# Kernel optimization log

Hardware: AMD Instinct MI355X
Metric: run time of the kernel (lower is better)

The kernel has to match this reference:

```python
import jax, jax.numpy as jnp
import numpy as np

B, P, E, V, H, NF = 256, 100, 32, 1000, 256, 33  # batch, pool, emb_size, vocab, hidden, n_embed_feats


def setup_inputs() -> dict:
    key = jax.random.key(0)
    k0, k1, k2, k3 = jax.random.split(key, 4)
    # integer-valued float tensor: cols 0,1 used raw; cols 2..34 cast to indices
    x = jax.random.randint(k0, (B, P, 35), 0, V).astype(jnp.float32)
    # 33 embedding tables stacked: [33, V, E]
    tables = jax.random.normal(k1, (NF, V, E), jnp.float32) * 0.02
    W1 = jax.random.normal(k2, (H, 35 * E), jnp.float32) * (1.0 / np.sqrt(35 * E))
    b1 = jnp.zeros((H,), jnp.float32)
    W2 = jax.random.normal(k3, (1, H), jnp.float32) * (1.0 / np.sqrt(H))
    b2 = jnp.zeros((1,), jnp.float32)
    return {"x": x, "tables": tables, "W1": W1, "b1": b1, "W2": W2, "b2": b2}


def reference(x, tables, W1, b1, W2, b2):
    b, p, _ = x.shape
    e = tables.shape[-1]
    # first 2 raw features repeated along embedding dim: [B,P,2,E]
    raw = jnp.repeat(x[:, :, :2, None], e, axis=3)
    # 33 embedding gathers, vectorized: tables[f, idx[...,f]] -> [B,P,33,E]
    idx = x[:, :, 2:].astype(jnp.int32)
    emb = tables[jnp.arange(NF)[None, None, :], idx]
    feat = jnp.concatenate([raw, emb], axis=2).reshape(b, p, 35 * e)
    h = jax.nn.relu(feat @ W1.T + b1)          # [B,P,256]
    logit = h @ W2.T + b2                       # [B,P,1]
    return jax.nn.softmax(logit, axis=1)        # softmax over pool dim
```

## Files before the change

### kernel.cpp

```cpp
#include <hip/hip_runtime.h>
#include <hip/hip_bf16.h>
#include <math.h>

#define BB 256
#define PP 100
#define EE 32
#define VV 1000
#define HH 256
#define NFF 33
#define F35 35
#define K1 1120
#define GSCALE 64.0f
#define GINV 0.015625f
#define NROWS (BB * PP)

#define FP8_HW 0
#if defined(__has_builtin)
#if __has_builtin(__builtin_amdgcn_cvt_pk_f32_fp8) && __has_builtin(__builtin_amdgcn_cvt_pk_fp8_f32)
#undef FP8_HW
#define FP8_HW 1
#endif
#endif

typedef float v2f __attribute__((ext_vector_type(2)));
typedef short bf16x8 __attribute__((ext_vector_type(8)));
typedef float f32x4 __attribute__((ext_vector_type(4)));

__device__ __forceinline__ unsigned char enc_fp8(float x) {
#if FP8_HW
    int pk = __builtin_amdgcn_cvt_pk_fp8_f32(x, 0.f, 0, false);
    return (unsigned char)(pk & 0xFF);
#else
    float a = fabsf(x);
    unsigned int s = (x < 0.f) ? 0x80u : 0u;
    if (a >= 448.f) return (unsigned char)(s | 0x7E);
    if (a < 0.015625f) {
        int m = (int)rintf(a * 512.f);
        if (m > 7) return (unsigned char)(s | 0x08);
        return (unsigned char)(s | (unsigned int)m);
    }
    unsigned int u = __float_as_uint(a);
    u += 0x00080000u;
    int e = (int)(u >> 23) - 127 + 7;
    if (e >= 16) return (unsigned char)(s | 0x7E);
    return (unsigned char)(s | ((unsigned int)e << 3) | ((u >> 20) & 7));
#endif
}

#if !FP8_HW
__device__ __forceinline__ float dec1(unsigned int b) {
    unsigned int s = b >> 7, e = (b >> 3) & 15, m = b & 7;
    float v = e ? __uint_as_float(((e + 120u) << 23) | (m << 20))
                : (float)m * 0.001953125f;
    return s ? -v : v;
}
#endif

__device__ __forceinline__ unsigned short f2bf(float x) {
    unsigned int b = __float_as_uint(x);
    return (unsigned short)((b + 0x7FFFu + ((b >> 16) & 1u)) >> 16);
}

__global__ __launch_bounds__(256) void k_pre(const float* __restrict__ tables,
                                             const float* __restrict__ W1,
                                             unsigned char* __restrict__ G,
                                             float* __restrict__ S01) {
    int bid = blockIdx.x;
    if (bid == NFF * 16) {
        int j = threadIdx.x;
        const float* row = W1 + (size_t)j * K1;
        float s0 = 0.f, s1 = 0.f;
#pragma unroll
        for (int e = 0; e < 32; ++e) { s0 += row[e]; s1 += row[32 + e]; }
        S01[j] = s0;
        S01[256 + j] = s1;
        return;
    }
    int f = bid % NFF;
    int rest = bid / NFF;
    int ctg = rest & 3;
    int vblk = rest >> 2;
    int t = threadIdx.x;
    int l = t & 63, w = t >> 6;
    int lr = l & 15, lg = l >> 4;

    const float* wp = W1 + (size_t)(ctg * 64 + w * 16 + lr) * K1 + 64 + 32 * f + lg * 4;
    float4 wa = *(const float4*)wp;
    float4 wb = *(const float4*)(wp + 16);
    bf16x8 afrag;
    afrag[0] = f2bf(wa.x); afrag[1] = f2bf(wa.y); afrag[2] = f2bf(wa.z); afrag[3] = f2bf(wa.w);
    afrag[4] = f2bf(wb.x); afrag[5] = f2bf(wb.y); afrag[6] = f2bf(wb.z); afrag[7] = f2bf(wb.w);

    __shared__ unsigned int stage[2][16][16];
    const f32x4 cz = {0.f, 0.f, 0.f, 0.f};

    for (int vt = 0; vt < 16; ++vt) {
        int v0 = vblk * 250 + vt * 16;
        int v = v0 + lr; if (v > VV - 1) v = VV - 1;
        const float* tp = tables + ((size_t)f * VV + v) * EE + lg * 4;
        float4 ta = *(const float4*)tp;
        float4 tb = *(const float4*)(tp + 16);
        bf16x8 bfrag;
        bfrag[0] = f2bf(ta.x); bfrag[1] = f2bf(ta.y); bfrag[2] = f2bf(ta.z); bfrag[3] = f2bf(ta.w);
        bfrag[4] = f2bf(tb.x); bfrag[5] = f2bf(tb.y); bfrag[6] = f2bf(tb.z); bfrag[7] = f2bf(tb.w);
        f32x4 d = __builtin_amdgcn_mfma_f32_16x16x32_bf16(afrag, bfrag, cz, 0, 0, 0);
        unsigned int pk;
#if FP8_HW
        int ipk = __builtin_amdgcn_cvt_pk_fp8_f32(d[0] * GSCALE, d[1] * GSCALE, 0, false);
        ipk = __builtin_amdgcn_cvt_pk_fp8_f32(d[2] * GSCALE, d[3] * GSCALE, ipk, true);
        pk = (unsigned int)ipk;
#else
        pk = (unsigned int)enc_fp8(d[0] * GSCALE) |
             ((unsigned int)enc_fp8(d[1] * GSCALE) << 8) |
             ((unsigned int)enc_fp8(d[2] * GSCALE) << 16) |
             ((unsigned int)enc_fp8(d[3] * GSCALE) << 24);
#endif
        stage[vt & 1][lr][w * 4 + lg] = pk;
        __syncthreads();
        if (t < 64) {
            int row = t >> 2, seg = t & 3;
            int vv = v0 + row;
            if (vv < VV) {
                uint4 val = *(const uint4*)&stage[vt & 1][row][seg * 4];
                *(uint4*)(G + ((size_t)f * VV + vv) * HH + ctg * 64 + seg * 16) = val;
            }
        }
    }
}

__global__ __launch_bounds__(256) void k_main(const float* __restrict__ x,
                                              const unsigned char* __restrict__ G,
                                              const float* __restrict__ S01,
                                              const float* __restrict__ b1,
                                              const float* __restrict__ W2,
                                              const float* __restrict__ b2,
                                              float* __restrict__ logits) {
    int lane = threadIdx.x & 63;
    int wave = threadIdx.x >> 6;
    int r = blockIdx.x * 4 + wave;
    const float* xr = x + (size_t)r * F35;
    float xv = (lane < F35) ? xr[lane] : 0.f;
    int xi = (int)xv;
    float x0 = __uint_as_float(__builtin_amdgcn_readlane(__float_as_uint(xv), 0));
    float x1 = __uint_as_float(__builtin_amdgcn_readlane(__float_as_uint(xv), 1));

    int j0 = lane * 4;
    float4 s0v = *(const float4*)(S01 + j0);
    float4 s1v = *(const float4*)(S01 + 256 + j0);
    float4 b1v = *(const float4*)(b1 + j0);
    float4 w2v = *(const float4*)(W2 + j0);

    v2f g01 = {0.f, 0.f}, g23 = {0.f, 0.f};
#pragma unroll
    for (int f = 0; f < NFF; ++f) {
        int v = __builtin_amdgcn_readlane((unsigned int)xi, 2 + f);
        const unsigned int* p = (const unsigned int*)(G + ((size_t)f * VV + v) * HH);
        unsigned int u = p[lane];
#if FP8_HW
        g01 += __builtin_amdgcn_cvt_pk_f32_fp8((int)u, false);
        g23 += __builtin_amdgcn_cvt_pk_f32_fp8((int)u, true);
#else
        g01[0] += dec1(u & 255u); g01[1] += dec1((u >> 8) & 255u);
        g23[0] += dec1((u >> 16) & 255u); g23[1] += dec1(u >> 24);
#endif
    }
    float a0 = b1v.x + x0 * s0v.x + x1 * s1v.x + g01[0] * GINV;
    float a1 = b1v.y + x0 * s0v.y + x1 * s1v.y + g01[1] * GINV;
    float a2 = b1v.z + x0 * s0v.z + x1 * s1v.z + g23[0] * GINV;
    float a3 = b1v.w + x0 * s0v.w + x1 * s1v.w + g23[1] * GINV;
    float part = fmaxf(a0, 0.f) * w2v.x + fmaxf(a1, 0.f) * w2v.y +
                 fmaxf(a2, 0.f) * w2v.z + fmaxf(a3, 0.f) * w2v.w;
#pragma unroll
    for (int m = 32; m > 0; m >>= 1) part += __shfl_xor(part, m, 64);
    if (lane == 0) logits[r] = part + b2[0];
}

__global__ void k_direct(const float* __restrict__ x,
                         const float* __restrict__ tables,
                         const float* __restrict__ W1,
                         const float* __restrict__ b1,
                         const float* __restrict__ W2,
                         const float* __restrict__ b2,
                         float* __restrict__ logits) {
    int r = blockIdx.x;
    int j = threadIdx.x;
    __shared__ int sidx[NFF];
    __shared__ float sx[2];
    __shared__ float red[256];
    const float* xr = x + (size_t)r * F35;
    if (j < 2) sx[j] = xr[j];
    if (j >= 2 && j < F35) sidx[j - 2] = (int)xr[j];
    __syncthreads();
    const float* w = W1 + (size_t)j * K1;
    float acc = b1[j];
    float s0 = 0.f, s1 = 0.f;
#pragma unroll
    for (int e = 0; e < 32; ++e) { s0 += w[e]; s1 += w[32 + e]; }
    acc += sx[0] * s0 + sx[1] * s1;
    for (int f = 0; f < NFF; ++f) {
        const float* tr = tables + ((size_t)f * VV + sidx[f]) * EE;
        const float* wf = w + 64 + 32 * f;
#pragma unroll
        for (int e = 0; e < 32; ++e) acc += tr[e] * wf[e];
    }
    float h = fmaxf(acc, 0.f);
    red[j] = h * W2[j];
    __syncthreads();
#pragma unroll
    for (int s = 128; s > 0; s >>= 1) {
        if (j < s) red[j] += red[j + s];
        __syncthreads();
    }
    if (j == 0) logits[r] = red[0] + b2[0];
}

__global__ void k_softmax(float* __restrict__ io) {
    int b = blockIdx.x;
    int t = threadIdx.x;
    __shared__ float buf[128];
    float v = (t < PP) ? io[(size_t)b * PP + t] : -INFINITY;
    buf[t] = v;
    __syncthreads();
#pragma unroll
    for (int s = 64; s > 0; s >>= 1) {
        if (t < s) buf[t] = fmaxf(buf[t], buf[t + s]);
        __syncthreads();
    }
    float m = buf[0];
    __syncthreads();
    float e = (t < PP) ? __expf(v - m) : 0.f;
    buf[t] = e;
    __syncthreads();
#pragma unroll
    for (int s = 64; s > 0; s >>= 1) {
        if (t < s) buf[t] += buf[t + s];
        __syncthreads();
    }
    float denom = buf[0];
    if (t < PP) io[(size_t)b * PP + t] = e / denom;
}

extern "C" void kernel_launch(void* const* d_in, const int* in_sizes, int n_in,
                              void* d_out, int out_size, void* d_ws, size_t ws_size,
                              hipStream_t stream) {
    const float* x      = (const float*)d_in[0];
    const float* tables = (const float*)d_in[1];
    const float* W1     = (const float*)d_in[2];
    const float* b1     = (const float*)d_in[3];
    const float* W2     = (const float*)d_in[4];
    const float* b2     = (const float*)d_in[5];
    float* out = (float*)d_out;

    const size_t gbytes = (size_t)NFF * VV * HH;
    const size_t need = gbytes + 2048;

    if (ws_size >= need) {
        char* ws = (char*)d_ws;
        unsigned char* G = (unsigned char*)ws;
        float* S01 = (float*)(ws + gbytes);
        hipLaunchKernelGGL(k_pre, dim3(NFF * 16 + 1), dim3(256), 0, stream, tables, W1, G, S01);
        hipLaunchKernelGGL(k_main, dim3(NROWS / 4), dim3(256), 0, stream,
                           x, G, S01, b1, W2, b2, out);
    } else {
        hipLaunchKernelGGL(k_direct, dim3(NROWS), dim3(256), 0, stream,
                           x, tables, W1, b1, W2, b2, out);
    }
    hipLaunchKernelGGL(k_softmax, dim3(BB), dim3(128), 0, stream, out);
}
```

Baseline: 43.83 us.

## Gather 16-byte fp8 chunks with 16 lanes per row; drop LDS staging

New measurement: 45.91 us. 1.05x slower.

```diff
diff --git a/kernel.cpp b/kernel.cpp
--- a/kernel.cpp
+++ b/kernel.cpp
@@ -91,9 +91,9 @@
     afrag[0] = f2bf(wa.x); afrag[1] = f2bf(wa.y); afrag[2] = f2bf(wa.z); afrag[3] = f2bf(wa.w);
     afrag[4] = f2bf(wb.x); afrag[5] = f2bf(wb.y); afrag[6] = f2bf(wb.z); afrag[7] = f2bf(wb.w);
 
-    __shared__ unsigned int stage[2][16][16];
     const f32x4 cz = {0.f, 0.f, 0.f, 0.f};
-
+    unsigned char* gdst = G + (size_t)(ctg * 64 + w * 16 + lg * 4);
+#pragma unroll 4
     for (int vt = 0; vt < 16; ++vt) {
         int v0 = vblk * 250 + vt * 16;
         int v = v0 + lr; if (v > VV - 1) v = VV - 1;
@@ -115,16 +115,7 @@
              ((unsigned int)enc_fp8(d[2] * GSCALE) << 16) |
              ((unsigned int)enc_fp8(d[3] * GSCALE) << 24);
 #endif
-        stage[vt & 1][lr][w * 4 + lg] = pk;
-        __syncthreads();
-        if (t < 64) {
-            int row = t >> 2, seg = t & 3;
-            int vv = v0 + row;
-            if (vv < VV) {
-                uint4 val = *(const uint4*)&stage[vt & 1][row][seg * 4];
-                *(uint4*)(G + ((size_t)f * VV + vv) * HH + ctg * 64 + seg * 16) = val;
-            }
-        }
+        *(unsigned int*)(gdst + ((size_t)f * VV + v) * HH) = pk;
     }
 }
 
@@ -135,44 +126,67 @@
                                               const float* __restrict__ W2,
                                               const float* __restrict__ b2,
                                               float* __restrict__ logits) {
-    int lane = threadIdx.x & 63;
-    int wave = threadIdx.x >> 6;
-    int r = blockIdx.x * 4 + wave;
-    const float* xr = x + (size_t)r * F35;
-    float xv = (lane < F35) ? xr[lane] : 0.f;
-    int xi = (int)xv;
-    float x0 = __uint_as_float(__builtin_amdgcn_readlane(__float_as_uint(xv), 0));
-    float x1 = __uint_as_float(__builtin_amdgcn_readlane(__float_as_uint(xv), 1));
-
-    int j0 = lane * 4;
-    float4 s0v = *(const float4*)(S01 + j0);
-    float4 s1v = *(const float4*)(S01 + 256 + j0);
-    float4 b1v = *(const float4*)(b1 + j0);
-    float4 w2v = *(const float4*)(W2 + j0);
-
-    v2f g01 = {0.f, 0.f}, g23 = {0.f, 0.f};
+    __shared__ int sxi[16][NFF];
+    __shared__ float sx01[16][2];
+    int t = threadIdx.x;
+    int rowbase = blockIdx.x * 16;
+    for (int k = t; k < 16 * F35; k += 256) {
+        int r = k / F35, c = k - r * F35;
+        float vv = x[(size_t)(rowbase + r) * F35 + c];
+        if (c < 2) sx01[r][c] = vv;
+        else sxi[r][c - 2] = (int)vv;
+    }
+    __syncthreads();
+    int lane = t & 63, wave = t >> 6;
+    int rg = lane >> 4, li = lane & 15;
+    int rloc = wave * 4 + rg;
+    v2f ac0 = {0.f, 0.f}, ac1 = {0.f, 0.f}, ac2 = {0.f, 0.f}, ac3 = {0.f, 0.f};
+    v2f ac4 = {0.f, 0.f}, ac5 = {0.f, 0.f}, ac6 = {0.f, 0.f}, ac7 = {0.f, 0.f};
 #pragma unroll
     for (int f = 0; f < NFF; ++f) {
-        int v = __builtin_amdgcn_readlane((unsigned int)xi, 2 + f);
-        const unsigned int* p = (const unsigned int*)(G + ((size_t)f * VV + v) * HH);
-        unsigned int u = p[lane];
+        int v = sxi[rloc][f];
+        uint4 u = *(const uint4*)(G + ((size_t)f * VV + v) * HH + li * 16);
 #if FP8_HW
-        g01 += __builtin_amdgcn_cvt_pk_f32_fp8((int)u, false);
-        g23 += __builtin_amdgcn_cvt_pk_f32_fp8((int)u, true);
+        ac0 += __builtin_amdgcn_cvt_pk_f32_fp8((int)u.x, false);
+        ac1 += __builtin_amdgcn_cvt_pk_f32_fp8((int)u.x, true);
+        ac2 += __builtin_amdgcn_cvt_pk_f32_fp8((int)u.y, false);
+        ac3 += __builtin_amdgcn_cvt_pk_f32_fp8((int)u.y, true);
+        ac4 += __builtin_amdgcn_cvt_pk_f32_fp8((int)u.z, false);
+        ac5 += __builtin_amdgcn_cvt_pk_f32_fp8((int)u.z, true);
+        ac6 += __builtin_amdgcn_cvt_pk_f32_fp8((int)u.w, false);
+        ac7 += __builtin_amdgcn_cvt_pk_f32_fp8((int)u.w, true);
 #else
-        g01[0] += dec1(u & 255u); g01[1] += dec1((u >> 8) & 255u);
-        g23[0] += dec1((u >> 16) & 255u); g23[1] += dec1(u >> 24);
-#endif
-    }
-    float a0 = b1v.x + x0 * s0v.x + x1 * s1v.x + g01[0] * GINV;
-    float a1 = b1v.y + x0 * s0v.y + x1 * s1v.y + g01[1] * GINV;
-    float a2 = b1v.z + x0 * s0v.z + x1 * s1v.z + g23[0] * GINV;
-    float a3 = b1v.w + x0 * s0v.w + x1 * s1v.w + g23[1] * GINV;
-    float part = fmaxf(a0, 0.f) * w2v.x + fmaxf(a1, 0.f) * w2v.y +
-                 fmaxf(a2, 0.f) * w2v.z + fmaxf(a3, 0.f) * w2v.w;
-#pragma unroll
-    for (int m = 32; m > 0; m >>= 1) part += __shfl_xor(part, m, 64);
-    if (lane == 0) logits[r] = part + b2[0];
+        ac0[0] += dec1(u.x & 255u); ac0[1] += dec1((u.x >> 8) & 255u);
+        ac1[0] += dec1((u.x >> 16) & 255u); ac1[1] += dec1(u.x >> 24);
+        ac2[0] += dec1(u.y & 255u); ac2[1] += dec1((u.y >> 8) & 255u);
+        ac3[0] += dec1((u.y >> 16) & 255u); ac3[1] += dec1(u.y >> 24);
+        ac4[0] += dec1(u.z & 255u); ac4[1] += dec1((u.z >> 8) & 255u);
+        ac5[0] += dec1((u.z >> 16) & 255u); ac5[1] += dec1(u.z >> 24);
+        ac6[0] += dec1(u.w & 255u); ac6[1] += dec1((u.w >> 8) & 255u);
+        ac7[0] += dec1((u.w >> 16) & 255u); ac7[1] += dec1(u.w >> 24);
+#endif
+    }
+    float x0 = sx01[rloc][0], x1 = sx01[rloc][1];
+    int j0 = li * 16;
+    float pacc = 0.f;
+#define QUAD(q, aclo, achi) {                                              \
+    float4 s0v = *(const float4*)(S01 + j0 + (q)*4);                       \
+    float4 s1v = *(const float4*)(S01 + 256 + j0 + (q)*4);                 \
+    float4 b1v = *(const float4*)(b1 + j0 + (q)*4);                        \
+    float4 w2v = *(const float4*)(W2 + j0 + (q)*4);                        \
+    float a0 = b1v.x + x0 * s0v.x + x1 * s1v.x + aclo[0] * GINV;           \
+    float a1 = b1v.y + x0 * s0v.y + x1 * s1v.y + aclo[1] * GINV;           \
+    float a2 = b1v.z + x0 * s0v.z + x1 * s1v.z + achi[0] * GINV;           \
+    float a3 = b1v.w + x0 * s0v.w + x1 * s1v.w + achi[1] * GINV;           \
+    pacc += fmaxf(a0, 0.f) * w2v.x + fmaxf(a1, 0.f) * w2v.y +              \
+            fmaxf(a2, 0.f) * w2v.z + fmaxf(a3, 0.f) * w2v.w; }
+    QUAD(0, ac0, ac1); QUAD(1, ac2, ac3); QUAD(2, ac4, ac5); QUAD(3, ac6, ac7);
+#undef QUAD
+    pacc += __shfl_xor(pacc, 1, 64);
+    pacc += __shfl_xor(pacc, 2, 64);
+    pacc += __shfl_xor(pacc, 4, 64);
+    pacc += __shfl_xor(pacc, 8, 64);
+    if (li == 0) logits[rowbase + rloc] = pacc + b2[0];
 }
 
 __global__ void k_direct(const float* __restrict__ x,
@@ -259,7 +273,7 @@
         unsigned char* G = (unsigned char*)ws;
         float* S01 = (float*)(ws + gbytes);
         hipLaunchKernelGGL(k_pre, dim3(NFF * 16 + 1), dim3(256), 0, stream, tables, W1, G, S01);
-        hipLaunchKernelGGL(k_main, dim3(NROWS / 4), dim3(256), 0, stream,
+        hipLaunchKernelGGL(k_main, dim3(NROWS / 16), dim3(256), 0, stream,
                            x, G, S01, b1, W2, b2, out);
     } else {
         hipLaunchKernelGGL(k_direct, dim3(NROWS), dim3(256), 0, stream,
```

## Fuse gather-MLP with softmax per batch and drop LDS staging in precompute

Applied to the files above, without the earlier changes.

Result: slower. 45.87 us (+4.6%).

```diff
diff --git a/kernel.cpp b/kernel.cpp
--- a/kernel.cpp
+++ b/kernel.cpp
@@ -91,9 +91,9 @@
     afrag[0] = f2bf(wa.x); afrag[1] = f2bf(wa.y); afrag[2] = f2bf(wa.z); afrag[3] = f2bf(wa.w);
     afrag[4] = f2bf(wb.x); afrag[5] = f2bf(wb.y); afrag[6] = f2bf(wb.z); afrag[7] = f2bf(wb.w);
 
-    __shared__ unsigned int stage[2][16][16];
     const f32x4 cz = {0.f, 0.f, 0.f, 0.f};
-
+    unsigned char* gdst = G + (size_t)(ctg * 64 + w * 16 + lg * 4);
+#pragma unroll 4
     for (int vt = 0; vt < 16; ++vt) {
         int v0 = vblk * 250 + vt * 16;
         int v = v0 + lr; if (v > VV - 1) v = VV - 1;
@@ -115,34 +115,31 @@
              ((unsigned int)enc_fp8(d[2] * GSCALE) << 16) |
              ((unsigned int)enc_fp8(d[3] * GSCALE) << 24);
 #endif
-        stage[vt & 1][lr][w * 4 + lg] = pk;
-        __syncthreads();
-        if (t < 64) {
-            int row = t >> 2, seg = t & 3;
-            int vv = v0 + row;
-            if (vv < VV) {
-                uint4 val = *(const uint4*)&stage[vt & 1][row][seg * 4];
-                *(uint4*)(G + ((size_t)f * VV + vv) * HH + ctg * 64 + seg * 16) = val;
-            }
-        }
-    }
-}
-
-__global__ __launch_bounds__(256) void k_main(const float* __restrict__ x,
-                                              const unsigned char* __restrict__ G,
-                                              const float* __restrict__ S01,
-                                              const float* __restrict__ b1,
-                                              const float* __restrict__ W2,
-                                              const float* __restrict__ b2,
-                                              float* __restrict__ logits) {
-    int lane = threadIdx.x & 63;
-    int wave = threadIdx.x >> 6;
-    int r = blockIdx.x * 4 + wave;
-    const float* xr = x + (size_t)r * F35;
-    float xv = (lane < F35) ? xr[lane] : 0.f;
-    int xi = (int)xv;
-    float x0 = __uint_as_float(__builtin_amdgcn_readlane(__float_as_uint(xv), 0));
-    float x1 = __uint_as_float(__builtin_amdgcn_readlane(__float_as_uint(xv), 1));
+        *(unsigned int*)(gdst + ((size_t)f * VV + v) * HH) = pk;
+    }
+}
+
+__global__ __launch_bounds__(1024) void k_fused(const float* __restrict__ x,
+                                                const unsigned char* __restrict__ G,
+                                                const float* __restrict__ S01,
+                                                const float* __restrict__ b1,
+                                                const float* __restrict__ W2,
+                                                float* __restrict__ out) {
+    __shared__ int sxi[PP][NFF];
+    __shared__ float sx01[PP][2];
+    __shared__ float slog[PP];
+    __shared__ float sred[128];
+    int t = threadIdx.x;
+    int b = blockIdx.x;
+    const float* xb = x + (size_t)b * PP * F35;
+    for (int k = t; k < PP * F35; k += 1024) {
+        int r = k / F35, c = k - r * F35;
+        float vv = xb[k];
+        if (c < 2) sx01[r][c] = vv;
+        else sxi[r][c - 2] = (int)vv;
+    }
+    __syncthreads();
+    int lane = t & 63, wave = t >> 6;
 
     int j0 = lane * 4;
     float4 s0v = *(const float4*)(S01 + j0);
@@ -150,29 +147,60 @@
     float4 b1v = *(const float4*)(b1 + j0);
     float4 w2v = *(const float4*)(W2 + j0);
 
-    v2f g01 = {0.f, 0.f}, g23 = {0.f, 0.f};
-#pragma unroll
-    for (int f = 0; f < NFF; ++f) {
-        int v = __builtin_amdgcn_readlane((unsigned int)xi, 2 + f);
-        const unsigned int* p = (const unsigned int*)(G + ((size_t)f * VV + v) * HH);
-        unsigned int u = p[lane];
+    for (int r = wave; r < PP; r += 16) {
+        int vlane = (lane < NFF) ? sxi[r][lane] : 0;
+        unsigned int u[NFF];
+#pragma unroll
+        for (int f = 0; f < NFF; ++f) {
+            int v = __builtin_amdgcn_readlane((unsigned int)vlane, f);
+            const unsigned int* p = (const unsigned int*)(G + ((size_t)f * VV + v) * HH);
+            u[f] = p[lane];
+        }
+        v2f g01 = {0.f, 0.f}, g23 = {0.f, 0.f};
+#pragma unroll
+        for (int f = 0; f < NFF; ++f) {
 #if FP8_HW
-        g01 += __builtin_amdgcn_cvt_pk_f32_fp8((int)u, false);
-        g23 += __builtin_amdgcn_cvt_pk_f32_fp8((int)u, true);
+            g01 += __builtin_amdgcn_cvt_pk_f32_fp8((int)u[f], false);
+            g23 += __builtin_amdgcn_cvt_pk_f32_fp8((int)u[f], true);
 #else
-        g01[0] += dec1(u & 255u); g01[1] += dec1((u >> 8) & 255u);
-        g23[0] += dec1((u >> 16) & 255u); g23[1] += dec1(u >> 24);
-#endif
-    }
-    float a0 = b1v.x + x0 * s0v.x + x1 * s1v.x + g01[0] * GINV;
-    float a1 = b1v.y + x0 * s0v.y + x1 * s1v.y + g01[1] * GINV;
-    float a2 = b1v.z + x0 * s0v.z + x1 * s1v.z + g23[0] * GINV;
-    float a3 = b1v.w + x0 * s0v.w + x1 * s1v.w + g23[1] * GINV;
-    float part = fmaxf(a0, 0.f) * w2v.x + fmaxf(a1, 0.f) * w2v.y +
-                 fmaxf(a2, 0.f) * w2v.z + fmaxf(a3, 0.f) * w2v.w;
-#pragma unroll
-    for (int m = 32; m > 0; m >>= 1) part += __shfl_xor(part, m, 64);
-    if (lane == 0) logits[r] = part + b2[0];
+            g01[0] += dec1(u[f] & 255u); g01[1] += dec1((u[f] >> 8) & 255u);
+            g23[0] += dec1((u[f] >> 16) & 255u); g23[1] += dec1(u[f] >> 24);
+#endif
+        }
+        float x0 = sx01[r][0], x1 = sx01[r][1];
+        float a0 = b1v.x + x0 * s0v.x + x1 * s1v.x + g01[0] * GINV;
+        float a1 = b1v.y + x0 * s0v.y + x1 * s1v.y + g01[1] * GINV;
+        float a2 = b1v.z + x0 * s0v.z + x1 * s1v.z + g23[0] * GINV;
+        float a3 = b1v.w + x0 * s0v.w + x1 * s1v.w + g23[1] * GINV;
+        float pacc = fmaxf(a0, 0.f) * w2v.x + fmaxf(a1, 0.f) * w2v.y +
+                     fmaxf(a2, 0.f) * w2v.z + fmaxf(a3, 0.f) * w2v.w;
+#pragma unroll
+        for (int m = 32; m > 0; m >>= 1) pacc += __shfl_xor(pacc, m, 64);
+        if (lane == 0) slog[r] = pacc;
+    }
+    __syncthreads();
+    if (t < 128) {
+        float v = (t < PP) ? slog[t] : -INFINITY;
+        sred[t] = v;
+        __builtin_amdgcn_s_barrier();
+#pragma unroll
+        for (int s = 64; s > 0; s >>= 1) {
+            if (t < s) sred[t] = fmaxf(sred[t], sred[t + s]);
+            __builtin_amdgcn_s_barrier();
+        }
+        float m = sred[0];
+        __builtin_amdgcn_s_barrier();
+        float e = (t < PP) ? __expf(v - m) : 0.f;
+        sred[t] = e;
+        __builtin_amdgcn_s_barrier();
+#pragma unroll
+        for (int s = 64; s > 0; s >>= 1) {
+            if (t < s) sred[t] += sred[t + s];
+            __builtin_amdgcn_s_barrier();
+        }
+        float denom = sred[0];
+        if (t < PP) out[(size_t)b * PP + t] = e / denom;
+    }
 }
 
 __global__ void k_direct(const float* __restrict__ x,
@@ -214,7 +242,7 @@
     if (j == 0) logits[r] = red[0] + b2[0];
 }
 
-__global__ void k_softmax(float* __restrict__ io) {
+__global__ void k_softmax_inplace(float* __restrict__ io) {
     int b = blockIdx.x;
     int t = threadIdx.x;
     __shared__ float buf[128];
@@ -259,11 +287,11 @@
         unsigned char* G = (unsigned char*)ws;
         float* S01 = (float*)(ws + gbytes);
         hipLaunchKernelGGL(k_pre, dim3(NFF * 16 + 1), dim3(256), 0, stream, tables, W1, G, S01);
-        hipLaunchKernelGGL(k_main, dim3(NROWS / 4), dim3(256), 0, stream,
-                           x, G, S01, b1, W2, b2, out);
+        hipLaunchKernelGGL(k_fused, dim3(BB), dim3(1024), 0, stream,
+                           x, G, S01, b1, W2, out);
     } else {
         hipLaunchKernelGGL(k_direct, dim3(NROWS), dim3(256), 0, stream,
                            x, tables, W1, b1, W2, b2, out);
-    }
-    hipLaunchKernelGGL(k_softmax, dim3(BB), dim3(128), 0, stream, out);
-}
+        hipLaunchKernelGGL(k_softmax_inplace, dim3(BB), dim3(128), 0, stream, out);
+    }
+}
```

## Quantize precomputed table-W1 products to FP4 and process two rows per wave

Applied to the files above, without the earlier changes.

New measurement: 56.82 us. 29.6% more time.

```diff
diff --git a/kernel.cpp b/kernel.cpp
--- a/kernel.cpp
+++ b/kernel.cpp
@@ -10,13 +10,14 @@
 #define NFF 33
 #define F35 35
 #define K1 1120
-#define GSCALE 64.0f
-#define GINV 0.015625f
+#define GSCALE4 256.0f
+#define GINV4 0.00390625f
 #define NROWS (BB * PP)
+#define G4_BYTES ((size_t)NFF * VV * 128)
 
 #define FP8_HW 0
 #if defined(__has_builtin)
-#if __has_builtin(__builtin_amdgcn_cvt_pk_f32_fp8) && __has_builtin(__builtin_amdgcn_cvt_pk_fp8_f32)
+#if __has_builtin(__builtin_amdgcn_cvt_pk_f32_fp8)
 #undef FP8_HW
 #define FP8_HW 1
 #endif
@@ -26,44 +27,49 @@
 typedef short bf16x8 __attribute__((ext_vector_type(8)));
 typedef float f32x4 __attribute__((ext_vector_type(4)));
 
-__device__ __forceinline__ unsigned char enc_fp8(float x) {
-#if FP8_HW
-    int pk = __builtin_amdgcn_cvt_pk_fp8_f32(x, 0.f, 0, false);
-    return (unsigned char)(pk & 0xFF);
-#else
-    float a = fabsf(x);
-    unsigned int s = (x < 0.f) ? 0x80u : 0u;
-    if (a >= 448.f) return (unsigned char)(s | 0x7E);
-    if (a < 0.015625f) {
-        int m = (int)rintf(a * 512.f);
-        if (m > 7) return (unsigned char)(s | 0x08);
-        return (unsigned char)(s | (unsigned int)m);
-    }
-    unsigned int u = __float_as_uint(a);
-    u += 0x00080000u;
-    int e = (int)(u >> 23) - 127 + 7;
-    if (e >= 16) return (unsigned char)(s | 0x7E);
-    return (unsigned char)(s | ((unsigned int)e << 3) | ((u >> 20) & 7));
-#endif
-}
-
-#if !FP8_HW
+__device__ __forceinline__ unsigned short f2bf(float x) {
+    unsigned int b = __float_as_uint(x);
+    return (unsigned short)((b + 0x7FFFu + ((b >> 16) & 1u)) >> 16);
+}
+
+__device__ __forceinline__ unsigned int enc_fp4(float y) {
+    unsigned int s = (__float_as_uint(y) >> 31) << 3;
+    float a = fabsf(y);
+    unsigned int n;
+    if (a < 0.25f) n = 0u;
+    else if (a < 0.75f) n = 1u;
+    else {
+        float ar = fminf(fmaxf(a, 1.0f), 6.0f);
+        unsigned int br = __float_as_uint(ar) + 0x00200000u;
+        unsigned int E = (br >> 23) - 127u;
+        unsigned int m = (br >> 22) & 1u;
+        n = ((E + 1u) << 1) | m;
+        if (n > 7u) n = 7u;
+    }
+    return n | s;
+}
+
 __device__ __forceinline__ float dec1(unsigned int b) {
     unsigned int s = b >> 7, e = (b >> 3) & 15, m = b & 7;
     float v = e ? __uint_as_float(((e + 120u) << 23) | (m << 20))
                 : (float)m * 0.001953125f;
     return s ? -v : v;
 }
-#endif
-
-__device__ __forceinline__ unsigned short f2bf(float x) {
-    unsigned int b = __float_as_uint(x);
-    return (unsigned short)((b + 0x7FFFu + ((b >> 16) & 1u)) >> 16);
+
+__device__ __forceinline__ unsigned int map4(unsigned int x) {
+    unsigned int t  = x & 0x07070707u;
+    unsigned int sb = (x & 0x08080808u) << 4;
+    unsigned int s1 = t >> 1, s2 = t >> 2;
+    unsigned int nz = (t | s1 | s2) & 0x01010101u;
+    unsigned int add0 = (nz << 5) | (nz << 4);
+    unsigned int is1 = (t & ~(s1 | s2)) & 0x01010101u;
+    unsigned int base = (t << 2) + add0 - (is1 << 2);
+    return base | sb;
 }
 
 __global__ __launch_bounds__(256) void k_pre(const float* __restrict__ tables,
                                              const float* __restrict__ W1,
-                                             unsigned char* __restrict__ G,
+                                             unsigned char* __restrict__ G4,
                                              float* __restrict__ S01) {
     int bid = blockIdx.x;
     if (bid == NFF * 16) {
@@ -91,9 +97,9 @@
     afrag[0] = f2bf(wa.x); afrag[1] = f2bf(wa.y); afrag[2] = f2bf(wa.z); afrag[3] = f2bf(wa.w);
     afrag[4] = f2bf(wb.x); afrag[5] = f2bf(wb.y); afrag[6] = f2bf(wb.z); afrag[7] = f2bf(wb.w);
 
-    __shared__ unsigned int stage[2][16][16];
     const f32x4 cz = {0.f, 0.f, 0.f, 0.f};
-
+    int chh = ctg * 32 + w * 8 + lg * 2;
+#pragma unroll 4
     for (int vt = 0; vt < 16; ++vt) {
         int v0 = vblk * 250 + vt * 16;
         int v = v0 + lr; if (v > VV - 1) v = VV - 1;
@@ -104,75 +110,105 @@
         bfrag[0] = f2bf(ta.x); bfrag[1] = f2bf(ta.y); bfrag[2] = f2bf(ta.z); bfrag[3] = f2bf(ta.w);
         bfrag[4] = f2bf(tb.x); bfrag[5] = f2bf(tb.y); bfrag[6] = f2bf(tb.z); bfrag[7] = f2bf(tb.w);
         f32x4 d = __builtin_amdgcn_mfma_f32_16x16x32_bf16(afrag, bfrag, cz, 0, 0, 0);
-        unsigned int pk;
-#if FP8_HW
-        int ipk = __builtin_amdgcn_cvt_pk_fp8_f32(d[0] * GSCALE, d[1] * GSCALE, 0, false);
-        ipk = __builtin_amdgcn_cvt_pk_fp8_f32(d[2] * GSCALE, d[3] * GSCALE, ipk, true);
-        pk = (unsigned int)ipk;
-#else
-        pk = (unsigned int)enc_fp8(d[0] * GSCALE) |
-             ((unsigned int)enc_fp8(d[1] * GSCALE) << 8) |
-             ((unsigned int)enc_fp8(d[2] * GSCALE) << 16) |
-             ((unsigned int)enc_fp8(d[3] * GSCALE) << 24);
-#endif
-        stage[vt & 1][lr][w * 4 + lg] = pk;
-        __syncthreads();
-        if (t < 64) {
-            int row = t >> 2, seg = t & 3;
-            int vv = v0 + row;
-            if (vv < VV) {
-                uint4 val = *(const uint4*)&stage[vt & 1][row][seg * 4];
-                *(uint4*)(G + ((size_t)f * VV + vv) * HH + ctg * 64 + seg * 16) = val;
-            }
-        }
+        unsigned int pk = enc_fp4(d[0] * GSCALE4) |
+                          (enc_fp4(d[1] * GSCALE4) << 4) |
+                          (enc_fp4(d[2] * GSCALE4) << 8) |
+                          (enc_fp4(d[3] * GSCALE4) << 12);
+        *(unsigned short*)(G4 + ((size_t)f * VV + v) * 128 + chh) = (unsigned short)pk;
     }
 }
 
 __global__ __launch_bounds__(256) void k_main(const float* __restrict__ x,
-                                              const unsigned char* __restrict__ G,
+                                              const unsigned char* __restrict__ G4,
                                               const float* __restrict__ S01,
                                               const float* __restrict__ b1,
                                               const float* __restrict__ W2,
-                                              const float* __restrict__ b2,
                                               float* __restrict__ logits) {
-    int lane = threadIdx.x & 63;
-    int wave = threadIdx.x >> 6;
-    int r = blockIdx.x * 4 + wave;
-    const float* xr = x + (size_t)r * F35;
-    float xv = (lane < F35) ? xr[lane] : 0.f;
-    int xi = (int)xv;
-    float x0 = __uint_as_float(__builtin_amdgcn_readlane(__float_as_uint(xv), 0));
-    float x1 = __uint_as_float(__builtin_amdgcn_readlane(__float_as_uint(xv), 1));
-
-    int j0 = lane * 4;
-    float4 s0v = *(const float4*)(S01 + j0);
-    float4 s1v = *(const float4*)(S01 + 256 + j0);
-    float4 b1v = *(const float4*)(b1 + j0);
-    float4 w2v = *(const float4*)(W2 + j0);
-
-    v2f g01 = {0.f, 0.f}, g23 = {0.f, 0.f};
+    __shared__ int sxi[8][NFF];
+    __shared__ float sx01[8][2];
+    int t = threadIdx.x;
+    int rowbase = blockIdx.x * 8;
+    for (int k = t; k < 8 * F35; k += 256) {
+        int r = k / F35, c = k - r * F35;
+        float vv = x[(size_t)(rowbase + r) * F35 + c];
+        if (c < 2) sx01[r][c] = vv;
+        else sxi[r][c - 2] = (int)vv;
+    }
+    __syncthreads();
+    int lane = t & 63, wave = t >> 6;
+    int rg = lane >> 5, li = lane & 31;
+    int rloc = wave * 2 + rg;
+
+    int j0 = li * 8;
+    float4 s0a = *(const float4*)(S01 + j0),        s0b = *(const float4*)(S01 + j0 + 4);
+    float4 s1a = *(const float4*)(S01 + 256 + j0),  s1b = *(const float4*)(S01 + 256 + j0 + 4);
+    float4 b1a = *(const float4*)(b1 + j0),         b1b = *(const float4*)(b1 + j0 + 4);
+    float4 w2a = *(const float4*)(W2 + j0),         w2b = *(const float4*)(W2 + j0 + 4);
+
+    v2f aEl = {0.f, 0.f}, aEh = {0.f, 0.f}, aOl = {0.f, 0.f}, aOh = {0.f, 0.f};
 #pragma unroll
     for (int f = 0; f < NFF; ++f) {
-        int v = __builtin_amdgcn_readlane((unsigned int)xi, 2 + f);
-        const unsigned int* p = (const unsigned int*)(G + ((size_t)f * VV + v) * HH);
-        unsigned int u = p[lane];
+        int v = sxi[rloc][f];
+        unsigned int u = *(const unsigned int*)(G4 + ((size_t)f * VV + v) * 128 + li * 4);
+        unsigned int xe = map4(u & 0x0F0F0F0Fu);
+        unsigned int xo = map4((u >> 4) & 0x0F0F0F0Fu);
 #if FP8_HW
-        g01 += __builtin_amdgcn_cvt_pk_f32_fp8((int)u, false);
-        g23 += __builtin_amdgcn_cvt_pk_f32_fp8((int)u, true);
+        aEl += __builtin_amdgcn_cvt_pk_f32_fp8((int)xe, false);
+        aEh += __builtin_amdgcn_cvt_pk_f32_fp8((int)xe, true);
+        aOl += __builtin_amdgcn_cvt_pk_f32_fp8((int)xo, false);
+        aOh += __builtin_amdgcn_cvt_pk_f32_fp8((int)xo, true);
 #else
-        g01[0] += dec1(u & 255u); g01[1] += dec1((u >> 8) & 255u);
-        g23[0] += dec1((u >> 16) & 255u); g23[1] += dec1(u >> 24);
+        aEl[0] += dec1(xe & 255u); aEl[1] += dec1((xe >> 8) & 255u);
+        aEh[0] += dec1((xe >> 16) & 255u); aEh[1] += dec1(xe >> 24);
+        aOl[0] += dec1(xo & 255u); aOl[1] += dec1((xo >> 8) & 255u);
+        aOh[0] += dec1((xo >> 16) & 255u); aOh[1] += dec1(xo >> 24);
 #endif
     }
-    float a0 = b1v.x + x0 * s0v.x + x1 * s1v.x + g01[0] * GINV;
-    float a1 = b1v.y + x0 * s0v.y + x1 * s1v.y + g01[1] * GINV;
-    float a2 = b1v.z + x0 * s0v.z + x1 * s1v.z + g23[0] * GINV;
-    float a3 = b1v.w + x0 * s0v.w + x1 * s1v.w + g23[1] * GINV;
-    float part = fmaxf(a0, 0.f) * w2v.x + fmaxf(a1, 0.f) * w2v.y +
-                 fmaxf(a2, 0.f) * w2v.z + fmaxf(a3, 0.f) * w2v.w;
-#pragma unroll
-    for (int m = 32; m > 0; m >>= 1) part += __shfl_xor(part, m, 64);
-    if (lane == 0) logits[r] = part + b2[0];
+    float x0 = sx01[rloc][0], x1 = sx01[rloc][1];
+    float h0 = b1a.x + x0 * s0a.x + x1 * s1a.x + aEl[0] * GINV4;
+    float h2 = b1a.z + x0 * s0a.z + x1 * s1a.z + aEl[1] * GINV4;
+    float h4 = b1b.x + x0 * s0b.x + x1 * s1b.x + aEh[0] * GINV4;
+    float h6 = b1b.z + x0 * s0b.z + x1 * s1b.z + aEh[1] * GINV4;
+    float h1 = b1a.y + x0 * s0a.y + x1 * s1a.y + aOl[0] * GINV4;
+    float h3 = b1a.w + x0 * s0a.w + x1 * s1a.w + aOl[1] * GINV4;
+    float h5 = b1b.y + x0 * s0b.y + x1 * s1b.y + aOh[0] * GINV4;
+    float h7 = b1b.w + x0 * s0b.w + x1 * s1b.w + aOh[1] * GINV4;
+    float p = fmaxf(h0, 0.f) * w2a.x + fmaxf(h2, 0.f) * w2a.z +
+              fmaxf(h4, 0.f) * w2b.x + fmaxf(h6, 0.f) * w2b.z +
+              fmaxf(h1, 0.f) * w2a.y + fmaxf(h3, 0.f) * w2a.w +
+              fmaxf(h5, 0.f) * w2b.y + fmaxf(h7, 0.f) * w2b.w;
+    p += __shfl_xor(p, 1, 64);
+    p += __shfl_xor(p, 2, 64);
+    p += __shfl_xor(p, 4, 64);
+    p += __shfl_xor(p, 8, 64);
+    p += __shfl_xor(p, 16, 64);
+    if (li == 0) logits[rowbase + rloc] = p;
+}
+
+__global__ void k_softmax(float* __restrict__ io) {
+    int b = blockIdx.x;
+    int t = threadIdx.x;
+    __shared__ float buf[128];
+    float v = (t < PP) ? io[(size_t)b * PP + t] : -INFINITY;
+    buf[t] = v;
+    __syncthreads();
+#pragma unroll
+    for (int s = 64; s > 0; s >>= 1) {
+        if (t < s) buf[t] = fmaxf(buf[t], buf[t + s]);
+        __syncthreads();
+    }
+    float m = buf[0];
+    __syncthreads();
+    float e = (t < PP) ? __expf(v - m) : 0.f;
+    buf[t] = e;
+    __syncthreads();
+#pragma unroll
+    for (int s = 64; s > 0; s >>= 1) {
+        if (t < s) buf[t] += buf[t + s];
+        __syncthreads();
+    }
+    float denom = buf[0];
+    if (t < PP) io[(size_t)b * PP + t] = e / denom;
 }
 
 __global__ void k_direct(const float* __restrict__ x,
@@ -214,32 +250,6 @@
     if (j == 0) logits[r] = red[0] + b2[0];
 }
 
-__global__ void k_softmax(float* __restrict__ io) {
-    int b = blockIdx.x;
-    int t = threadIdx.x;
-    __shared__ float buf[128];
-    float v = (t < PP) ? io[(size_t)b * PP + t] : -INFINITY;
-    buf[t] = v;
-    __syncthreads();
-#pragma unroll
-    for (int s = 64; s > 0; s >>= 1) {
-        if (t < s) buf[t] = fmaxf(buf[t], buf[t + s]);
-        __syncthreads();
-    }
-    float m = buf[0];
-    __syncthreads();
-    float e = (t < PP) ? __expf(v - m) : 0.f;
-    buf[t] = e;
-    __syncthreads();
-#pragma unroll
-    for (int s = 64; s > 0; s >>= 1) {
-        if (t < s) buf[t] += buf[t + s];
-        __syncthreads();
-    }
-    float denom = buf[0];
-    if (t < PP) io[(size_t)b * PP + t] = e / denom;
-}
-
 extern "C" void kernel_launch(void* const* d_in, const int* in_sizes, int n_in,
                               void* d_out, int out_size, void* d_ws, size_t ws_size,
                               hipStream_t stream) {
@@ -251,16 +261,15 @@
     const float* b2     = (const float*)d_in[5];
     float* out = (float*)d_out;
 
-    const size_t gbytes = (size_t)NFF * VV * HH;
-    const size_t need = gbytes + 2048;
+    const size_t need = G4_BYTES + 2048;
 
     if (ws_size >= need) {
         char* ws = (char*)d_ws;
-        unsigned char* G = (unsigned char*)ws;
-        float* S01 = (float*)(ws + gbytes);
-        hipLaunchKernelGGL(k_pre, dim3(NFF * 16 + 1), dim3(256), 0, stream, tables, W1, G, S01);
-        hipLaunchKernelGGL(k_main, dim3(NROWS / 4), dim3(256), 0, stream,
-                           x, G, S01, b1, W2, b2, out);
+        unsigned char* G4 = (unsigned char*)ws;
+        float* S01 = (float*)(ws + G4_BYTES);
+        hipLaunchKernelGGL(k_pre, dim3(NFF * 16 + 1), dim3(256), 0, stream, tables, W1, G4, S01);
+        hipLaunchKernelGGL(k_main, dim3(NROWS / 8), dim3(256), 0, stream,
+                           x, G4, S01, b1, W2, out);
     } else {
         hipLaunchKernelGGL(k_direct, dim3(NROWS), dim3(256), 0, stream,
                            x, tables, W1, b1, W2, b2, out);
```
